# Performance work log

Hardware: AMD Instinct MI355X
Metric: run time of the kernel (lower is better)

## Reference

```python
import jax, jax.numpy as jnp
import numpy as np

B, U = 64, 512          # batch, max_units
CORE, UNIT = 512, 256   # core_output_size, unit_embedding_size
HID, ACT = 1024, 12     # hidden_layer_size, ACTION_COUNT


def setup_inputs() -> dict:
    key = jax.random.key(0)
    ks = jax.random.split(key, 6)
    core_output = jax.random.normal(ks[0], (B, 1, CORE), dtype=jnp.float32)
    own_unit_embeddings = jax.random.normal(ks[1], (B, U, UNIT), dtype=jnp.float32)
    nr_units = jax.random.randint(ks[2], (B, 1), 0, U, dtype=jnp.int32)
    nr_own_flags = jax.random.randint(ks[3], (B, 1), 0, 64, dtype=jnp.int32)
    W1 = jax.random.normal(ks[4], (CORE + UNIT, HID), dtype=jnp.float32) * (1.0 / np.sqrt(CORE + UNIT))
    b1 = jnp.zeros((HID,), dtype=jnp.float32)
    W2 = jax.random.normal(ks[5], (HID, ACT), dtype=jnp.float32) * (1.0 / np.sqrt(HID))
    b2 = jnp.zeros((ACT,), dtype=jnp.float32)
    return {"core_output": core_output, "own_unit_embeddings": own_unit_embeddings,
            "nr_units": nr_units, "nr_own_flags": nr_own_flags,
            "W1": W1, "b1": b1, "W2": W2, "b2": b2}


def reference(core_output, own_unit_embeddings, nr_units, nr_own_flags, W1, b1, W2, b2):
    b, u, _ = own_unit_embeddings.shape
    # broadcast core output to every unit slot and concat along features: [B, U, UNIT+CORE]
    core_rep = jnp.broadcast_to(core_output, (b, u, core_output.shape[-1]))
    combined = jnp.concatenate([own_unit_embeddings, core_rep], axis=-1)
    autoregressive_embedding = jax.nn.relu(jnp.einsum('buf,fh->buh', combined, W1) + b1)
    logits = jnp.einsum('buh,ha->bua', autoregressive_embedding, W2) + b2
    action_probs = jax.nn.softmax(logits, axis=-1)
    # vectorized range mask: mask[i, f:n, :] = 1 else 1e-9
    idx = jnp.arange(u, dtype=nr_units.dtype)[None, :]        # [1, U]
    valid = (idx >= nr_own_flags) & (idx < nr_units)          # [B, U]
    mask = jnp.where(valid, 1.0, 1e-9).astype(action_probs.dtype)[:, :, None]
    return action_probs * mask, autoregressive_embedding
```

## Files before the change

### kernel.cpp

```cpp
#include <hip/hip_runtime.h>
#include <hip/hip_fp16.h>
#include <cstdint>

typedef unsigned short ushort_t;
typedef _Float16 f16x8 __attribute__((ext_vector_type(8)));
typedef float f32x4 __attribute__((ext_vector_type(4)));

#define M_TOT  32768
#define K_EMB  256
#define K_CORE 512
#define ACT    12

__device__ __forceinline__ unsigned int pack2h(float a, float b) {
    __half2 h = __floats2half2_rn(a, b);
    union { __half2 h2; unsigned int u; } v; v.h2 = h; return v.u;
}

__global__ __launch_bounds__(256) void transpose_k(const float* __restrict__ W1,
                                                   ushort_t* __restrict__ W1T) {
    __shared__ float tile[64][65];
    const int t = threadIdx.x;
    const int k0 = blockIdx.x * 64, n0 = blockIdx.y * 64;
    const int r = t >> 4, c4 = (t & 15) * 4;
#pragma unroll
    for (int p = 0; p < 4; ++p) {
        const int row = r + p * 16;
        const float4 v = *(const float4*)(W1 + (size_t)(k0 + row) * 1024 + n0 + c4);
        tile[row][c4 + 0] = v.x; tile[row][c4 + 1] = v.y;
        tile[row][c4 + 2] = v.z; tile[row][c4 + 3] = v.w;
    }
    __syncthreads();
#pragma unroll
    for (int p = 0; p < 4; ++p) {
        const int nrow = r + p * 16;
        uint2 o;
        o.x = pack2h(tile[c4 + 0][nrow], tile[c4 + 1][nrow]);
        o.y = pack2h(tile[c4 + 2][nrow], tile[c4 + 3][nrow]);
        *(uint2*)(W1T + (size_t)(n0 + nrow) * 256 + k0 + c4) = o;
    }
}

__global__ __launch_bounds__(256) void corepart_k(const float* __restrict__ core,
                                                  const float* __restrict__ W1,
                                                  const float* __restrict__ b1,
                                                  float* __restrict__ cp) {
    const int b = blockIdx.y;
    const int n = blockIdx.x * 256 + threadIdx.x;
    float s = b1[n];
    const float* cr = core + b * K_CORE;
    const float* wp = W1 + (size_t)K_EMB * 1024 + n;
#pragma unroll 8
    for (int k = 0; k < K_CORE; ++k)
        s += cr[k] * wp[(size_t)k * 1024];
    cp[b * 1024 + n] = s;
}

__global__ __launch_bounds__(256, 1) void fused_k(const float* __restrict__ emb,
                                                  const ushort_t* __restrict__ w1t,
                                                  const float* __restrict__ cp,
                                                  const float* __restrict__ W2,
                                                  const float* __restrict__ b2,
                                                  const int* __restrict__ nr_units,
                                                  const int* __restrict__ nr_flags,
                                                  float* __restrict__ out0,
                                                  float* __restrict__ out1) {
    __shared__ __align__(16) ushort_t Asl[128 * 32];
    __shared__ __align__(16) ushort_t Bsl[128 * 32];
    __shared__ __align__(16) float logitAcc[128][ACT];

    const int t = threadIdx.x;
    const int w = t >> 6, L = t & 63;
    const int wm = w >> 1, wn = w & 1;
    const int lane16 = L & 15, qd = L >> 4;
    const int m0 = blockIdx.x * 128;
    const int bb = m0 >> 9;

    const int c0 = w * 128 + L, c1 = c0 + 64;
    const int rA0 = c0 >> 2, g0 = c0 & 3;
    const int rA1 = c1 >> 2, g1 = c1 & 3;
    uint4* lA0 = (uint4*)&Asl[rA0 * 32 + ((g0 ^ ((rA0 >> 1) & 3)) << 3)];
    uint4* lA1 = (uint4*)&Asl[rA1 * 32 + ((g1 ^ ((rA1 >> 1) & 3)) << 3)];
    uint4* lB0 = (uint4*)&Bsl[rA0 * 32 + ((g0 ^ ((rA0 >> 1) & 3)) << 3)];
    uint4* lB1 = (uint4*)&Bsl[rA1 * 32 + ((g1 ^ ((rA1 >> 1) & 3)) << 3)];
    const float*    gA0 = emb + (size_t)(m0 + rA0) * K_EMB + g0 * 8;
    const float*    gA1 = emb + (size_t)(m0 + rA1) * K_EMB + g1 * 8;
    const ushort_t* gB0 = w1t + (size_t)rA0 * K_EMB + g0 * 8;
    const ushort_t* gB1 = w1t + (size_t)rA1 * K_EMB + g1 * 8;

    int aoff[4], boff[4];
#pragma unroll
    for (int i = 0; i < 4; ++i) {
        const int ra = wm * 64 + i * 16 + lane16;
        aoff[i] = ra * 32 + ((qd ^ ((ra >> 1) & 3)) << 3);
        const int rb = wn * 64 + i * 16 + lane16;
        boff[i] = rb * 32 + ((qd ^ ((rb >> 1) & 3)) << 3);
    }

    f32x4 acc[4][4];
#pragma unroll
    for (int mi = 0; mi < 4; ++mi)
#pragma unroll
        for (int ni = 0; ni < 4; ++ni) acc[mi][ni] = (f32x4){0.f, 0.f, 0.f, 0.f};
    f32x4 la_a[16], la_b[16], la_c[16];
#pragma unroll
    for (int i = 0; i < 16; ++i) {
        la_a[i] = (f32x4){0.f, 0.f, 0.f, 0.f};
        la_b[i] = (f32x4){0.f, 0.f, 0.f, 0.f};
        la_c[i] = (f32x4){0.f, 0.f, 0.f, 0.f};
    }

    float4 pa0l = *(const float4*)gA0, pa0h = *(const float4*)(gA0 + 4);
    float4 pa1l = *(const float4*)gA1, pa1h = *(const float4*)(gA1 + 4);
    uint4  pb0  = *(const uint4*)gB0,  pb1  = *(const uint4*)gB1;

    for (int it = 0; it < 64; ++it) {
        if (it) __syncthreads();
        uint4 av0, av1;
        av0.x = pack2h(pa0l.x, pa0l.y); av0.y = pack2h(pa0l.z, pa0l.w);
        av0.z = pack2h(pa0h.x, pa0h.y); av0.w = pack2h(pa0h.z, pa0h.w);
        av1.x = pack2h(pa1l.x, pa1l.y); av1.y = pack2h(pa1l.z, pa1l.w);
        av1.z = pack2h(pa1h.x, pa1h.y); av1.w = pack2h(pa1h.z, pa1h.w);
        *lA0 = av0; *lA1 = av1; *lB0 = pb0; *lB1 = pb1;
        __syncthreads();
        if (it < 63) {
            const int itn = it + 1;
            const int ksn = itn & 7, ntn = itn >> 3;
            const size_t ao = (size_t)(ksn * 32);
            const size_t bo = (size_t)ntn * 128 * K_EMB + ksn * 32;
            pa0l = *(const float4*)(gA0 + ao); pa0h = *(const float4*)(gA0 + ao + 4);
            pa1l = *(const float4*)(gA1 + ao); pa1h = *(const float4*)(gA1 + ao + 4);
            pb0 = *(const uint4*)(gB0 + bo);   pb1 = *(const uint4*)(gB1 + bo);
        }
        f16x8 af[4], bfr[4];
#pragma unroll
        for (int mi = 0; mi < 4; ++mi) af[mi] = *(const f16x8*)&Asl[aoff[mi]];
#pragma unroll
        for (int ni = 0; ni < 4; ++ni) bfr[ni] = *(const f16x8*)&Bsl[boff[ni]];
#pragma unroll
        for (int mi = 0; mi < 4; ++mi)
#pragma unroll
            for (int ni = 0; ni < 4; ++ni)
                acc[mi][ni] = __builtin_amdgcn_mfma_f32_16x16x32_f16(af[mi], bfr[ni], acc[mi][ni], 0, 0, 0);

        if ((it & 7) == 7) {
            const int nt = it >> 3;
            const int colb = nt * 128 + wn * 64 + lane16;
            float cpv[4]; f32x4 w2a[4], w2b[4], w2c[4];
#pragma unroll
            for (int ni = 0; ni < 4; ++ni) {
                const int cg = colb + ni * 16;
                cpv[ni] = cp[bb * 1024 + cg];
                const f32x4* wp = (const f32x4*)(W2 + (size_t)cg * ACT);
                w2a[ni] = wp[0]; w2b[ni] = wp[1]; w2c[ni] = wp[2];
            }
#pragma unroll
            for (int mi = 0; mi < 4; ++mi) {
#pragma unroll
                for (int r = 0; r < 4; ++r) {
                    const size_t m = (size_t)(m0 + wm * 64 + mi * 16 + qd * 4 + r);
                    float* orow = out1 + m * 1024 + colb;
#pragma unroll
                    for (int ni = 0; ni < 4; ++ni) {
                        float v = acc[mi][ni][r] + cpv[ni];
                        v = v > 0.f ? v : 0.f;
                        orow[ni * 16] = v;
                        la_a[mi * 4 + r] += w2a[ni] * v;
                        la_b[mi * 4 + r] += w2b[ni] * v;
                        la_c[mi * 4 + r] += w2c[ni] * v;
                    }
                }
#pragma unroll
                for (int ni = 0; ni < 4; ++ni) acc[mi][ni] = (f32x4){0.f, 0.f, 0.f, 0.f};
            }
        }
    }

#pragma unroll
    for (int i = 0; i < 16; ++i)
#pragma unroll
        for (int s = 1; s < 16; s <<= 1)
#pragma unroll
            for (int j = 0; j < 4; ++j) {
                la_a[i][j] += __shfl_xor(la_a[i][j], s, 64);
                la_b[i][j] += __shfl_xor(la_b[i][j], s, 64);
                la_c[i][j] += __shfl_xor(la_c[i][j], s, 64);
            }

    __syncthreads();
    if (wn == 0 && lane16 == 0) {
#pragma unroll
        for (int i = 0; i < 16; ++i) {
            const int row = wm * 64 + (i >> 2) * 16 + qd * 4 + (i & 3);
            f32x4* p = (f32x4*)&logitAcc[row][0];
            p[0] = la_a[i]; p[1] = la_b[i]; p[2] = la_c[i];
        }
    }
    __syncthreads();
    if (wn == 1 && lane16 == 0) {
#pragma unroll
        for (int i = 0; i < 16; ++i) {
            const int row = wm * 64 + (i >> 2) * 16 + qd * 4 + (i & 3);
            f32x4* p = (f32x4*)&logitAcc[row][0];
            p[0] += la_a[i]; p[1] += la_b[i]; p[2] += la_c[i];
        }
    }
    __syncthreads();

    if (t < 128) {
        float lg[ACT];
#pragma unroll
        for (int a = 0; a < ACT; ++a) lg[a] = logitAcc[t][a] + b2[a];
        float mx = lg[0];
#pragma unroll
        for (int a = 1; a < ACT; ++a) mx = fmaxf(mx, lg[a]);
        float s = 0.f;
#pragma unroll
        for (int a = 0; a < ACT; ++a) { lg[a] = __expf(lg[a] - mx); s += lg[a]; }
        const float inv = 1.f / s;
        const int m = m0 + t;
        const int u = m & 511;
        const float msk = (u >= nr_flags[bb] && u < nr_units[bb]) ? 1.0f : 1e-9f;
        f32x4* op = (f32x4*)(out0 + (size_t)m * ACT);
        f32x4 o0, o1, o2;
#pragma unroll
        for (int j = 0; j < 4; ++j) {
            o0[j] = lg[j] * inv * msk;
            o1[j] = lg[j + 4] * inv * msk;
            o2[j] = lg[j + 8] * inv * msk;
        }
        op[0] = o0; op[1] = o1; op[2] = o2;
    }
}

extern "C" void kernel_launch(void* const* d_in, const int* in_sizes, int n_in,
                              void* d_out, int out_size, void* d_ws, size_t ws_size,
                              hipStream_t stream) {
    const float* core   = (const float*)d_in[0];
    const float* emb    = (const float*)d_in[1];
    const int* nr_units = (const int*)d_in[2];
    const int* nr_flags = (const int*)d_in[3];
    const float* W1     = (const float*)d_in[4];
    const float* b1     = (const float*)d_in[5];
    const float* W2     = (const float*)d_in[6];
    const float* b2     = (const float*)d_in[7];

    float* out0 = (float*)d_out;
    float* out1 = out0 + (size_t)M_TOT * ACT;

    ushort_t* w1t = (ushort_t*)d_ws;
    float* cp = (float*)((char*)d_ws + (size_t)1024 * 256 * 2);

    transpose_k<<<dim3(4, 16), 256, 0, stream>>>(W1, w1t);
    corepart_k<<<dim3(4, 64), 256, 0, stream>>>(core, W1, b1, cp);
    fused_k<<<dim3(256), 256, 0, stream>>>(emb, w1t, cp, W2, b2, nr_units, nr_flags, out0, out1);
}
```

Baseline: 267.4 us.

## Shrink fused tile to 32 rows, keep A resident in LDS, stream B from registers

```diff
diff --git a/kernel.cpp b/kernel.cpp
--- a/kernel.cpp
+++ b/kernel.cpp
@@ -10,11 +10,13 @@
 #define K_EMB  256
 #define K_CORE 512
 #define ACT    12
+#define AP     264
 
 __device__ __forceinline__ unsigned int pack2h(float a, float b) {
     __half2 h = __floats2half2_rn(a, b);
     union { __half2 h2; unsigned int u; } v; v.h2 = h; return v.u;
 }
+union U4H { uint4 u; f16x8 h; };
 
 __global__ __launch_bounds__(256) void transpose_k(const float* __restrict__ W1,
                                                    ushort_t* __restrict__ W1T) {
@@ -55,7 +57,7 @@
     cp[b * 1024 + n] = s;
 }
 
-__global__ __launch_bounds__(256, 1) void fused_k(const float* __restrict__ emb,
+__global__ __launch_bounds__(256, 4) void fused_k(const float* __restrict__ emb,
                                                   const ushort_t* __restrict__ w1t,
                                                   const float* __restrict__ cp,
                                                   const float* __restrict__ W2,
@@ -64,103 +66,81 @@
                                                   const int* __restrict__ nr_flags,
                                                   float* __restrict__ out0,
                                                   float* __restrict__ out1) {
-    __shared__ __align__(16) ushort_t Asl[128 * 32];
-    __shared__ __align__(16) ushort_t Bsl[128 * 32];
-    __shared__ __align__(16) float logitAcc[128][ACT];
+    __shared__ __align__(16) ushort_t Af[32 * AP];
+    __shared__ __align__(16) float parts[4][32][ACT];
 
     const int t = threadIdx.x;
     const int w = t >> 6, L = t & 63;
-    const int wm = w >> 1, wn = w & 1;
     const int lane16 = L & 15, qd = L >> 4;
-    const int m0 = blockIdx.x * 128;
+    const int m0 = blockIdx.x * 32;
     const int bb = m0 >> 9;
 
-    const int c0 = w * 128 + L, c1 = c0 + 64;
-    const int rA0 = c0 >> 2, g0 = c0 & 3;
-    const int rA1 = c1 >> 2, g1 = c1 & 3;
-    uint4* lA0 = (uint4*)&Asl[rA0 * 32 + ((g0 ^ ((rA0 >> 1) & 3)) << 3)];
-    uint4* lA1 = (uint4*)&Asl[rA1 * 32 + ((g1 ^ ((rA1 >> 1) & 3)) << 3)];
-    uint4* lB0 = (uint4*)&Bsl[rA0 * 32 + ((g0 ^ ((rA0 >> 1) & 3)) << 3)];
-    uint4* lB1 = (uint4*)&Bsl[rA1 * 32 + ((g1 ^ ((rA1 >> 1) & 3)) << 3)];
-    const float*    gA0 = emb + (size_t)(m0 + rA0) * K_EMB + g0 * 8;
-    const float*    gA1 = emb + (size_t)(m0 + rA1) * K_EMB + g1 * 8;
-    const ushort_t* gB0 = w1t + (size_t)rA0 * K_EMB + g0 * 8;
-    const ushort_t* gB1 = w1t + (size_t)rA1 * K_EMB + g1 * 8;
-
-    int aoff[4], boff[4];
-#pragma unroll
-    for (int i = 0; i < 4; ++i) {
-        const int ra = wm * 64 + i * 16 + lane16;
-        aoff[i] = ra * 32 + ((qd ^ ((ra >> 1) & 3)) << 3);
-        const int rb = wn * 64 + i * 16 + lane16;
-        boff[i] = rb * 32 + ((qd ^ ((rb >> 1) & 3)) << 3);
-    }
-
-    f32x4 acc[4][4];
-#pragma unroll
-    for (int mi = 0; mi < 4; ++mi)
-#pragma unroll
-        for (int ni = 0; ni < 4; ++ni) acc[mi][ni] = (f32x4){0.f, 0.f, 0.f, 0.f};
-    f32x4 la_a[16], la_b[16], la_c[16];
-#pragma unroll
-    for (int i = 0; i < 16; ++i) {
+    const float* gA = emb + (size_t)m0 * K_EMB;
+#pragma unroll
+    for (int j = 0; j < 8; ++j) {
+        const int f = j * 256 + t;
+        const float4 v = *(const float4*)(gA + f * 4);
+        const int row = f >> 6, col = (f & 63) * 4;
+        uint2 o; o.x = pack2h(v.x, v.y); o.y = pack2h(v.z, v.w);
+        *(uint2*)&Af[row * AP + col] = o;
+    }
+    __syncthreads();
+
+    f32x4 acc[2][2];
+#pragma unroll
+    for (int mi = 0; mi < 2; ++mi)
+#pragma unroll
+        for (int ni = 0; ni < 2; ++ni) acc[mi][ni] = (f32x4){0.f, 0.f, 0.f, 0.f};
+    f32x4 la_a[8], la_b[8], la_c[8];
+#pragma unroll
+    for (int i = 0; i < 8; ++i) {
         la_a[i] = (f32x4){0.f, 0.f, 0.f, 0.f};
         la_b[i] = (f32x4){0.f, 0.f, 0.f, 0.f};
         la_c[i] = (f32x4){0.f, 0.f, 0.f, 0.f};
     }
 
-    float4 pa0l = *(const float4*)gA0, pa0h = *(const float4*)(gA0 + 4);
-    float4 pa1l = *(const float4*)gA1, pa1h = *(const float4*)(gA1 + 4);
-    uint4  pb0  = *(const uint4*)gB0,  pb1  = *(const uint4*)gB1;
-
+    const ushort_t* gB = w1t + (size_t)(w * 32 + lane16) * K_EMB + qd * 8;
+#define BOFF(IT, NI) ((((IT) >> 3) * 128 + (NI) * 16) * K_EMB + ((IT) & 7) * 32)
+
+    uint4 bp[2][2];
+    bp[0][0] = *(const uint4*)(gB + BOFF(0, 0));
+    bp[0][1] = *(const uint4*)(gB + BOFF(0, 1));
+    bp[1][0] = *(const uint4*)(gB + BOFF(1, 0));
+    bp[1][1] = *(const uint4*)(gB + BOFF(1, 1));
+
+#pragma unroll 8
     for (int it = 0; it < 64; ++it) {
-        if (it) __syncthreads();
-        uint4 av0, av1;
-        av0.x = pack2h(pa0l.x, pa0l.y); av0.y = pack2h(pa0l.z, pa0l.w);
-        av0.z = pack2h(pa0h.x, pa0h.y); av0.w = pack2h(pa0h.z, pa0h.w);
-        av1.x = pack2h(pa1l.x, pa1l.y); av1.y = pack2h(pa1l.z, pa1l.w);
-        av1.z = pack2h(pa1h.x, pa1h.y); av1.w = pack2h(pa1h.z, pa1h.w);
-        *lA0 = av0; *lA1 = av1; *lB0 = pb0; *lB1 = pb1;
-        __syncthreads();
-        if (it < 63) {
-            const int itn = it + 1;
-            const int ksn = itn & 7, ntn = itn >> 3;
-            const size_t ao = (size_t)(ksn * 32);
-            const size_t bo = (size_t)ntn * 128 * K_EMB + ksn * 32;
-            pa0l = *(const float4*)(gA0 + ao); pa0h = *(const float4*)(gA0 + ao + 4);
-            pa1l = *(const float4*)(gA1 + ao); pa1h = *(const float4*)(gA1 + ao + 4);
-            pb0 = *(const uint4*)(gB0 + bo);   pb1 = *(const uint4*)(gB1 + bo);
-        }
-        f16x8 af[4], bfr[4];
-#pragma unroll
-        for (int mi = 0; mi < 4; ++mi) af[mi] = *(const f16x8*)&Asl[aoff[mi]];
-#pragma unroll
-        for (int ni = 0; ni < 4; ++ni) bfr[ni] = *(const f16x8*)&Bsl[boff[ni]];
-#pragma unroll
-        for (int mi = 0; mi < 4; ++mi)
-#pragma unroll
-            for (int ni = 0; ni < 4; ++ni)
-                acc[mi][ni] = __builtin_amdgcn_mfma_f32_16x16x32_f16(af[mi], bfr[ni], acc[mi][ni], 0, 0, 0);
-
-        if ((it & 7) == 7) {
+        const int ks = it & 7;
+        U4H b0, b1; b0.u = bp[it & 1][0]; b1.u = bp[it & 1][1];
+        if (it + 2 < 64) {
+            bp[it & 1][0] = *(const uint4*)(gB + BOFF(it + 2, 0));
+            bp[it & 1][1] = *(const uint4*)(gB + BOFF(it + 2, 1));
+        }
+        f16x8 af0 = *(const f16x8*)&Af[(lane16)      * AP + ks * 32 + qd * 8];
+        f16x8 af1 = *(const f16x8*)&Af[(16 + lane16) * AP + ks * 32 + qd * 8];
+        acc[0][0] = __builtin_amdgcn_mfma_f32_16x16x32_f16(af0, b0.h, acc[0][0], 0, 0, 0);
+        acc[0][1] = __builtin_amdgcn_mfma_f32_16x16x32_f16(af0, b1.h, acc[0][1], 0, 0, 0);
+        acc[1][0] = __builtin_amdgcn_mfma_f32_16x16x32_f16(af1, b0.h, acc[1][0], 0, 0, 0);
+        acc[1][1] = __builtin_amdgcn_mfma_f32_16x16x32_f16(af1, b1.h, acc[1][1], 0, 0, 0);
+
+        if (ks == 7) {
             const int nt = it >> 3;
-            const int colb = nt * 128 + wn * 64 + lane16;
-            float cpv[4]; f32x4 w2a[4], w2b[4], w2c[4];
-#pragma unroll
-            for (int ni = 0; ni < 4; ++ni) {
-                const int cg = colb + ni * 16;
+            float cpv[2]; f32x4 w2a[2], w2b[2], w2c[2];
+#pragma unroll
+            for (int ni = 0; ni < 2; ++ni) {
+                const int cg = nt * 128 + w * 32 + ni * 16 + lane16;
                 cpv[ni] = cp[bb * 1024 + cg];
                 const f32x4* wp = (const f32x4*)(W2 + (size_t)cg * ACT);
                 w2a[ni] = wp[0]; w2b[ni] = wp[1]; w2c[ni] = wp[2];
             }
 #pragma unroll
-            for (int mi = 0; mi < 4; ++mi) {
+            for (int mi = 0; mi < 2; ++mi) {
 #pragma unroll
                 for (int r = 0; r < 4; ++r) {
-                    const size_t m = (size_t)(m0 + wm * 64 + mi * 16 + qd * 4 + r);
-                    float* orow = out1 + m * 1024 + colb;
-#pragma unroll
-                    for (int ni = 0; ni < 4; ++ni) {
+                    const size_t m = (size_t)(m0 + mi * 16 + qd * 4 + r);
+                    float* orow = out1 + m * 1024 + nt * 128 + w * 32 + lane16;
+#pragma unroll
+                    for (int ni = 0; ni < 2; ++ni) {
                         float v = acc[mi][ni][r] + cpv[ni];
                         v = v > 0.f ? v : 0.f;
                         orow[ni * 16] = v;
@@ -170,13 +150,14 @@
                     }
                 }
 #pragma unroll
-                for (int ni = 0; ni < 4; ++ni) acc[mi][ni] = (f32x4){0.f, 0.f, 0.f, 0.f};
+                for (int ni = 0; ni < 2; ++ni) acc[mi][ni] = (f32x4){0.f, 0.f, 0.f, 0.f};
             }
         }
     }
-
-#pragma unroll
-    for (int i = 0; i < 16; ++i)
+#undef BOFF
+
+#pragma unroll
+    for (int i = 0; i < 8; ++i)
 #pragma unroll
         for (int s = 1; s < 16; s <<= 1)
 #pragma unroll
@@ -185,31 +166,21 @@
                 la_b[i][j] += __shfl_xor(la_b[i][j], s, 64);
                 la_c[i][j] += __shfl_xor(la_c[i][j], s, 64);
             }
-
+    if (lane16 == 0) {
+#pragma unroll
+        for (int i = 0; i < 8; ++i) {
+            const int row = (i >> 2) * 16 + qd * 4 + (i & 3);
+            f32x4* p = (f32x4*)&parts[w][row][0];
+            p[0] = la_a[i]; p[1] = la_b[i]; p[2] = la_c[i];
+        }
+    }
     __syncthreads();
-    if (wn == 0 && lane16 == 0) {
-#pragma unroll
-        for (int i = 0; i < 16; ++i) {
-            const int row = wm * 64 + (i >> 2) * 16 + qd * 4 + (i & 3);
-            f32x4* p = (f32x4*)&logitAcc[row][0];
-            p[0] = la_a[i]; p[1] = la_b[i]; p[2] = la_c[i];
-        }
-    }
-    __syncthreads();
-    if (wn == 1 && lane16 == 0) {
-#pragma unroll
-        for (int i = 0; i < 16; ++i) {
-            const int row = wm * 64 + (i >> 2) * 16 + qd * 4 + (i & 3);
-            f32x4* p = (f32x4*)&logitAcc[row][0];
-            p[0] += la_a[i]; p[1] += la_b[i]; p[2] += la_c[i];
-        }
-    }
-    __syncthreads();
-
-    if (t < 128) {
+
+    if (t < 32) {
         float lg[ACT];
 #pragma unroll
-        for (int a = 0; a < ACT; ++a) lg[a] = logitAcc[t][a] + b2[a];
+        for (int a = 0; a < ACT; ++a)
+            lg[a] = parts[0][t][a] + parts[1][t][a] + parts[2][t][a] + parts[3][t][a] + b2[a];
         float mx = lg[0];
 #pragma unroll
         for (int a = 1; a < ACT; ++a) mx = fmaxf(mx, lg[a]);
@@ -252,5 +223,5 @@
 
     transpose_k<<<dim3(4, 16), 256, 0, stream>>>(W1, w1t);
     corepart_k<<<dim3(4, 64), 256, 0, stream>>>(core, W1, b1, cp);
-    fused_k<<<dim3(256), 256, 0, stream>>>(emb, w1t, cp, W2, b2, nr_units, nr_flags, out0, out1);
-}
+    fused_k<<<dim3(1024), 256, 0, stream>>>(emb, w1t, cp, W2, b2, nr_units, nr_flags, out0, out1);
+}
```

After: 511.3 us. +91.2%, slower.
